# Kernel tuning notes

Hardware: AMD Instinct MI355X
Metric: run time of the kernel (lower is better)

Reference implementation:

```python
import jax, jax.numpy as jnp
import numpy as np

BN_EPS = 1e-5


def conv1x1(x, w, b):
    # x: [B, C, H, W], w: [O, C], b: [O]
    return jnp.einsum('bchw,oc->bohw', x, w) + b[None, :, None, None]


def cca(x, wq, bq, wk, bk, wv, bv, wg, bg):
    # Criss-cross attention block: full HWxHW attention with qk dim = C//8
    B, C, H, W = x.shape
    N = H * W
    q = conv1x1(x, wq, bq).reshape(B, -1, N)   # [B, C//8, N]
    k = conv1x1(x, wk, bk).reshape(B, -1, N)   # [B, C//8, N]
    v = conv1x1(x, wv, bv).reshape(B, C, N)    # [B, C, N]
    att = jax.nn.softmax(jnp.einsum('bdq,bdk->bqk', q, k), axis=-1)  # [B, N, N]
    out = jnp.einsum('bck,bqk->bcq', v, att).reshape(B, C, H, W)
    return x + conv1x1(out, wg, bg)


def setup_inputs() -> dict:
    key = jax.random.key(0)
    ks = iter(jax.random.split(key, 64))

    def rn(shape, s=0.1):
        return jax.random.normal(next(ks), shape, dtype=jnp.float32) * s

    C_IN = [48, 96, 192, 384]
    OC = 8            # hardcoded out_channels in the module
    NOUT = 19         # num_outputs
    LC = OC * 4       # last_inp_channels
    d = {}
    d['x0'] = rn((2, 48, 96, 96), 1.0)
    d['x1'] = rn((2, 96, 48, 48), 1.0)
    d['x2'] = rn((2, 192, 24, 24), 1.0)
    d['x3'] = rn((2, 384, 12, 12), 1.0)
    for i, c in enumerate(C_IN):
        d[f'w{i}'] = rn((OC, c))
        d[f'b{i}'] = rn((OC,))
    # cca3 params are never used by the original forward (it calls cca1 on x_3),
    # so only cca0/cca1/cca2 are materialized.
    for i in range(3):
        d[f'cca{i}_wq'] = rn((OC // 8, OC)); d[f'cca{i}_bq'] = rn((OC // 8,))
        d[f'cca{i}_wk'] = rn((OC // 8, OC)); d[f'cca{i}_bk'] = rn((OC // 8,))
        d[f'cca{i}_wv'] = rn((OC, OC));      d[f'cca{i}_bv'] = rn((OC,))
        d[f'cca{i}_wg'] = rn((OC, OC));      d[f'cca{i}_bg'] = rn((OC,))
    d['wl0'] = rn((LC, LC)); d['bl0'] = rn((LC,))
    d['bn_s'] = jnp.ones((LC,), jnp.float32)
    d['bn_b'] = jnp.zeros((LC,), jnp.float32)
    d['bn_m'] = rn((LC,), 0.01)
    d['bn_v'] = jnp.ones((LC,), jnp.float32)
    d['wl1'] = rn((NOUT, LC)); d['bl1'] = rn((NOUT,))
    return d


def reference(x0, x1, x2, x3, w0, b0, w1, b1, w2, b2, w3, b3,
              cca0_wq, cca0_bq, cca0_wk, cca0_bk, cca0_wv, cca0_bv, cca0_wg, cca0_bg,
              cca1_wq, cca1_bq, cca1_wk, cca1_bk, cca1_wv, cca1_bv, cca1_wg, cca1_bg,
              cca2_wq, cca2_bq, cca2_wk, cca2_bk, cca2_wv, cca2_bv, cca2_wg, cca2_bg,
              wl0, bl0, bn_s, bn_b, bn_m, bn_v, wl1, bl1):
    y0 = cca(conv1x1(x0, w0, b0), cca0_wq, cca0_bq, cca0_wk, cca0_bk, cca0_wv, cca0_bv, cca0_wg, cca0_bg)
    y1 = cca(conv1x1(x1, w1, b1), cca1_wq, cca1_bq, cca1_wk, cca1_bk, cca1_wv, cca1_bv, cca1_wg, cca1_bg)
    y2 = cca(conv1x1(x2, w2, b2), cca2_wq, cca2_bq, cca2_wk, cca2_bk, cca2_wv, cca2_bv, cca2_wg, cca2_bg)
    # NOTE: original torch code applies cca1 (not cca3) to x_3 -- reproduced faithfully.
    y3 = cca(conv1x1(x3, w3, b3), cca1_wq, cca1_bq, cca1_wk, cca1_bk, cca1_wv, cca1_bv, cca1_wg, cca1_bg)

    B, C, H0, W0 = y0.shape

    def up(t):
        # torch F.interpolate(mode='bilinear', align_corners=False) == jax half-pixel bilinear
        return jax.image.resize(t, (t.shape[0], t.shape[1], H0, W0), method='bilinear')

    x = jnp.concatenate([y0, up(y1), up(y2), up(y3)], axis=1)  # [B, 32, H0, W0]
    x = conv1x1(x, wl0, bl0)
    scale = (bn_s / jnp.sqrt(bn_v + BN_EPS))[None, :, None, None]
    x = (x - bn_m[None, :, None, None]) * scale + bn_b[None, :, None, None]
    x = jax.nn.relu(x)
    return conv1x1(x, wl1, bl1)
```

## Files before the change

### kernel.cpp

```cpp
#include <hip/hip_runtime.h>
#include <math.h>

#define LB __launch_bounds__(256)

#define NSLOT 24480
#define MT 28
#define NMOM 252
#define NBLK_Q 540
#define NSLICE 4

typedef float f32x4 __attribute__((ext_vector_type(4)));

struct QkvmArgs {
  const float *x0, *x1, *x2, *x3;
  const float *w0, *w1, *w2, *w3;
  const float *c0, *c1, *c2, *c3;
  const float *wq[4], *bq[4], *wk[4], *bk[4], *wv[4], *bv[4];
  float *P, *Q;
  float *MOMP;
};

template<int CG>
__device__ __forceinline__ void qkvm_body(const QkvmArgs& a, const int scale, const int C,
    const int N, const int slotoff, const int rel,
    const float* __restrict__ xp, const float* __restrict__ wp, const float* __restrict__ bp,
    float* s_w, float* s_sm, float* s_red, float* s_kp, float* s_v) {
  constexpr int PX = 256 / CG;
  const int tid = threadIdx.x;
  const int bpb = N / PX;
  const int b = rel / bpb, blk = rel - b*bpb;
  const int px = tid & (PX - 1), cg = tid / PX;
  const int n = blk*PX + px;
  const float* xb = xp + (size_t)b*C*N + n;
  const int c0 = cg*12;
  float xv[12];
  #pragma unroll
  for (int cc = 0; cc < 12; ++cc) xv[cc] = xb[(size_t)(c0+cc)*N];

  for (int i = tid; i < 8*C; i += 256) { const int c = i >> 3, o = i & 7; s_w[i] = wp[o*C + c]; }
  if (tid >= 128 && tid < 192) { const int t = tid - 128; s_sm[32 + t] = a.wv[scale][(t & 7)*8 + (t >> 3)]; }
  if (tid < 8) {
    s_sm[tid]      = bp[tid];
    s_sm[8 + tid]  = a.wq[scale][tid];
    s_sm[16 + tid] = a.wk[scale][tid];
    s_sm[24 + tid] = a.bv[scale][tid];
  }
  if (tid == 96) { s_sm[96] = a.bq[scale][0]; s_sm[97] = a.bk[scale][0]; }
  __syncthreads();

  float p[8];
  #pragma unroll
  for (int o = 0; o < 8; ++o) p[o] = 0.f;
  #pragma unroll
  for (int cc = 0; cc < 12; ++cc) {
    const float x = xv[cc];
    #pragma unroll
    for (int o = 0; o < 8; ++o) p[o] = fmaf(s_w[(c0+cc)*8+o], x, p[o]);
  }
  f32x4* sp = (f32x4*)&s_red[tid*8];
  sp[0] = (f32x4){p[0], p[1], p[2], p[3]};
  sp[1] = (f32x4){p[4], p[5], p[6], p[7]};
  __syncthreads();

  if (tid < PX) {
    float pc[8];
    #pragma unroll
    for (int o = 0; o < 8; ++o) {
      float s = s_sm[o];
      #pragma unroll
      for (int g = 0; g < CG; ++g) s += s_red[(g*PX + tid)*8 + o];
      pc[o] = s;
    }
    float q = s_sm[96], kv = s_sm[97];
    #pragma unroll
    for (int c = 0; c < 8; ++c) { q = fmaf(s_sm[8+c], pc[c], q); kv = fmaf(s_sm[16+c], pc[c], kv); }
    float v[8];
    #pragma unroll
    for (int o = 0; o < 8; ++o) v[o] = s_sm[24 + o];
    #pragma unroll
    for (int c = 0; c < 8; ++c) {
      const float pcc = pc[c];
      #pragma unroll
      for (int o = 0; o < 8; ++o) v[o] = fmaf(s_sm[32 + c*8 + o], pcc, v[o]);
    }
    const int g = slotoff + b*N + n;
    f32x4* Pp = (f32x4*)&a.P[(size_t)g*8];
    Pp[0] = (f32x4){pc[0], pc[1], pc[2], pc[3]};
    Pp[1] = (f32x4){pc[4], pc[5], pc[6], pc[7]};
    a.Q[g] = q;
    s_kp[tid*MT] = 1.f;
    float pw = 1.f;
    #pragma unroll
    for (int m = 1; m < MT; ++m) { pw *= kv; s_kp[tid*MT + m] = pw; }
    #pragma unroll
    for (int j = 0; j < 8; ++j) s_v[tid*8 + j] = v[j];
  }
  __syncthreads();

  if (tid < NMOM) {
    const int m = tid / 9, j = tid - m*9;
    float acc = 0.f;
    if (j == 0) {
      #pragma unroll 8
      for (int e = 0; e < PX; ++e) acc += s_kp[e*MT + m];
    } else {
      #pragma unroll 8
      for (int e = 0; e < PX; ++e) acc = fmaf(s_kp[e*MT + m], s_v[e*8 + (j-1)], acc);
    }
    a.MOMP[(size_t)blockIdx.x*NMOM + tid] = acc;
  }
}

__global__ LB void qkvm_kernel(QkvmArgs a) {
  __shared__ __align__(16) float s_w[3072];
  __shared__ __align__(16) float s_sm[104];
  __shared__ __align__(16) float s_red[256*8];
  __shared__ __align__(16) float s_kp[64*MT];
  __shared__ __align__(16) float s_v[64*8];
  const int bid = blockIdx.x;
  if (bid < 288)      qkvm_body<4> (a, 0, 48,  9216, 0,     bid,     a.x0, a.w0, a.c0, s_w, s_sm, s_red, s_kp, s_v);
  else if (bid < 432) qkvm_body<8> (a, 1, 96,  2304, 18432, bid-288, a.x1, a.w1, a.c1, s_w, s_sm, s_red, s_kp, s_v);
  else if (bid < 504) qkvm_body<16>(a, 2, 192, 576,  23040, bid-432, a.x2, a.w2, a.c2, s_w, s_sm, s_red, s_kp, s_v);
  else                qkvm_body<32>(a, 3, 384, 144,  24192, bid-504, a.x3, a.w3, a.c3, s_w, s_sm, s_red, s_kp, s_v);
}

__global__ LB void momred_kernel(const float* __restrict__ MOMP, float* __restrict__ MOMQ) {
  const int sb = blockIdx.x / NSLICE, sl = blockIdx.x - sb*NSLICE;
  const int tid = threadIdx.x;
  if (tid >= NMOM) return;
  const int start[8] = {0, 144, 288, 360, 432, 468, 504, 522};
  const int cnt[8]   = {144, 144, 72, 72, 36, 36, 18, 18};
  const int r0 = start[sb] + (cnt[sb]*sl)/NSLICE;
  const int r1 = start[sb] + (cnt[sb]*(sl+1))/NSLICE;
  const float* bp = MOMP + (size_t)r0*NMOM + tid;
  const int c = r1 - r0;
  float a0=0.f,a1=0.f,a2=0.f,a3=0.f,a4=0.f,a5=0.f,a6=0.f,a7=0.f;
  int t = 0;
  for (; t + 8 <= c; t += 8) {
    a0 += bp[(size_t)(t+0)*NMOM];
    a1 += bp[(size_t)(t+1)*NMOM];
    a2 += bp[(size_t)(t+2)*NMOM];
    a3 += bp[(size_t)(t+3)*NMOM];
    a4 += bp[(size_t)(t+4)*NMOM];
    a5 += bp[(size_t)(t+5)*NMOM];
    a6 += bp[(size_t)(t+6)*NMOM];
    a7 += bp[(size_t)(t+7)*NMOM];
  }
  for (; t < c; ++t) a0 += bp[(size_t)t*NMOM];
  const float s = ((a0+a1)+(a2+a3)) + ((a4+a5)+(a6+a7));
  MOMQ[(size_t)blockIdx.x*NMOM + tid] = s;
}

__device__ __forceinline__ void taylor_eval(const float* __restrict__ mb, const float* __restrict__ wg,
                                            const float* __restrict__ bg8, const float q,
                                            const float* __restrict__ Pp, float* y) {
  float t = 1.f, den = 0.f;
  float num[8];
  #pragma unroll
  for (int c = 0; c < 8; ++c) num[c] = 0.f;
  #pragma unroll
  for (int m = 0; m < MT; ++m) {
    const f32x4 a0 = *(const f32x4*)&mb[m*12];
    const f32x4 a1 = *(const f32x4*)&mb[m*12 + 4];
    const f32x4 a2 = *(const f32x4*)&mb[m*12 + 8];
    den    = fmaf(t, a0.x, den);
    num[0] = fmaf(t, a0.y, num[0]); num[1] = fmaf(t, a0.z, num[1]); num[2] = fmaf(t, a0.w, num[2]);
    num[3] = fmaf(t, a1.x, num[3]); num[4] = fmaf(t, a1.y, num[4]); num[5] = fmaf(t, a1.z, num[5]);
    num[6] = fmaf(t, a1.w, num[6]); num[7] = fmaf(t, a2.x, num[7]);
    if (m + 1 < MT) t *= q * (1.f/(float)(m+1));
  }
  const float inv = 1.f/den;
  float o8[8];
  #pragma unroll
  for (int c = 0; c < 8; ++c) o8[c] = num[c]*inv;
  const f32x4 pA = *(const f32x4*)Pp;
  const f32x4 pB = *(const f32x4*)(Pp + 4);
  const float pv[8] = {pA.x, pA.y, pA.z, pA.w, pB.x, pB.y, pB.z, pB.w};
  #pragma unroll
  for (int o = 0; o < 8; ++o) {
    float s2 = pv[o] + bg8[o];
    #pragma unroll
    for (int c = 0; c < 8; ++c) s2 = fmaf(wg[o*8 + c], o8[c], s2);
    y[o] = s2;
  }
}

template<int HS>
__device__ __forceinline__ void bilerp_lds(float* zo, const float* __restrict__ sYb,
                                           const int r, const int h, const int w) {
  constexpr float inv = (float)HS/96.0f;
  const float sy = (h + 0.5f)*inv - 0.5f;
  const float sx = (w + 0.5f)*inv - 0.5f;
  const int iy0 = (int)floorf(sy); const float fy = sy - (float)iy0;
  const int ix0 = (int)floorf(sx); const float fx = sx - (float)ix0;
  const float syE = (2*r + 0.5f)*inv - 0.5f;
  const int ybase = (int)floorf(syE);
  const int ly0 = iy0 - ybase;
  const int x0 = min(max(ix0, 0), HS-1), x1 = min(max(ix0 + 1, 0), HS-1);
  const float* p00 = &sYb[((ly0  )*HS + x0)*8];
  const float* p01 = &sYb[((ly0  )*HS + x1)*8];
  const float* p10 = &sYb[((ly0+1)*HS + x0)*8];
  const float* p11 = &sYb[((ly0+1)*HS + x1)*8];
  const float w00 = (1.f-fy)*(1.f-fx), w01 = (1.f-fy)*fx, w10 = fy*(1.f-fx), w11 = fy*fx;
  #pragma unroll
  for (int c = 0; c < 8; ++c)
    zo[c] = w00*p00[c] + w01*p01[c] + w10*p10[c] + w11*p11[c];
}

struct HFArgs {
  const float *Q, *P, *MOMQ;
  const float *wg0, *bg0, *wg1, *bg1, *wg2, *bg2;
  const float *wl0, *bl0, *bn_s, *bn_b, *bn_m, *bn_v, *wl1, *bl1;
  float *out;
};

__global__ LB void headfin_kernel(HFArgs a) {
  __shared__ __align__(16) float smom[8*MT*12];
  __shared__ __align__(16) float sY[2016];
  __shared__ float swg[3][64], sbg[3][8];
  __shared__ float s_wl0[1024], s_wl1[608];
  __shared__ float s_bl0[32], s_sc[32], s_sh[32], s_bl1[19];
  const int tid = threadIdx.x;
  const int bid = blockIdx.x;
  const int b = bid / 48, r = bid - b*48;

  for (int i = tid; i < 1024; i += 256) s_wl0[i] = a.wl0[i];
  for (int i = tid; i < 608;  i += 256) s_wl1[i] = a.wl1[i];
  if (tid < 64) { swg[0][tid] = a.wg0[tid]; swg[1][tid] = a.wg1[tid]; swg[2][tid] = a.wg2[tid]; }
  if (tid < 8)  { sbg[0][tid] = a.bg0[tid]; sbg[1][tid] = a.bg1[tid]; sbg[2][tid] = a.bg2[tid]; }
  if (tid >= 64 && tid < 96) {
    const int c = tid - 64;
    s_bl0[c] = a.bl0[c];
    const float sc = a.bn_s[c] / sqrtf(a.bn_v[c] + 1e-5f);
    s_sc[c] = sc;
    s_sh[c] = a.bn_b[c] - a.bn_m[c]*sc;
  }
  if (tid >= 96 && tid < 115) s_bl1[tid - 96] = a.bl1[tid - 96];
  for (int i = tid; i < 8*MT*12; i += 256) {
    const int sbi = i / (MT*12), rr = i - sbi*(MT*12);
    const int m = rr / 12, j = rr - m*12;
    float s = 0.f;
    if (j < 9) {
      const float* qp = a.MOMQ + (size_t)sbi*NSLICE*NMOM + (m*9 + j);
      #pragma unroll
      for (int sl = 0; sl < NSLICE; ++sl) s += qp[(size_t)sl*NMOM];
    }
    smom[i] = s;
  }
  __syncthreads();

  if (tid < 252) {
    int HS, soff, Nc, sb, widx, base, row_i, x;
    if (tid < 144)      { HS=48; soff=18432; Nc=2304; sb=2+b; widx=1; base=0;    row_i=tid/48;       x=tid-48*(tid/48); }
    else if (tid < 216) { const int t=tid-144; HS=24; soff=23040; Nc=576; sb=4+b; widx=2; base=1152; row_i=t/24; x=t-24*(t/24); }
    else                { const int t=tid-216; HS=12; soff=24192; Nc=144; sb=6+b; widx=1; base=1728; row_i=t/12; x=t-12*(t/12); }
    const float syE = (2*r + 0.5f)*(float)HS/96.0f - 0.5f;
    const int ybase = (int)floorf(syE);
    const int row = min(max(ybase + row_i, 0), HS-1);
    const int slot = soff + b*Nc + row*HS + x;
    float y[8];
    taylor_eval(&smom[sb*(MT*12)], swg[widx], sbg[widx], a.Q[slot], &a.P[(size_t)slot*8], y);
    #pragma unroll
    for (int c = 0; c < 8; ++c) sY[base + (row_i*HS + x)*8 + c] = y[c];
  }
  __syncthreads();

  if (tid < 192) {
    const int hh = tid / 96;
    const int h = 2*r + hh;
    const int w = tid - 96*hh;
    const int n = h*96 + w;
    float z[32];
    {
      const int slot = b*9216 + n;
      taylor_eval(&smom[b*(MT*12)], swg[0], sbg[0], a.Q[slot], &a.P[(size_t)slot*8], z);
    }
    bilerp_lds<48>(z + 8,  &sY[0],    r, h, w);
    bilerp_lds<24>(z + 16, &sY[1152], r, h, w);
    bilerp_lds<12>(z + 24, &sY[1728], r, h, w);
    float o19[19];
    #pragma unroll
    for (int j = 0; j < 19; ++j) o19[j] = s_bl1[j];
    #pragma unroll 1
    for (int o = 0; o < 32; ++o) {
      float sA = s_bl0[o], sB = 0.f;
      #pragma unroll
      for (int c4 = 0; c4 < 4; ++c4) {
        const f32x4 wv = *(const f32x4*)&s_wl0[o*32 + c4*4];
        sA = fmaf(wv.x, z[c4*4+0], sA);
        sA = fmaf(wv.y, z[c4*4+1], sA);
        sA = fmaf(wv.z, z[c4*4+2], sA);
        sA = fmaf(wv.w, z[c4*4+3], sA);
      }
      #pragma unroll
      for (int c4 = 4; c4 < 8; ++c4) {
        const f32x4 wv = *(const f32x4*)&s_wl0[o*32 + c4*4];
        sB = fmaf(wv.x, z[c4*4+0], sB);
        sB = fmaf(wv.y, z[c4*4+1], sB);
        sB = fmaf(wv.z, z[c4*4+2], sB);
        sB = fmaf(wv.w, z[c4*4+3], sB);
      }
      const float t = fmaxf(fmaf(sA + sB, s_sc[o], s_sh[o]), 0.f);
      #pragma unroll
      for (int j = 0; j < 19; ++j) o19[j] = fmaf(s_wl1[j*32 + o], t, o19[j]);
    }
    #pragma unroll
    for (int j = 0; j < 19; ++j)
      a.out[((size_t)b*19 + j)*9216 + n] = o19[j];
  }
}

extern "C" void kernel_launch(void* const* d_in, const int* in_sizes, int n_in,
                              void* d_out, int out_size, void* d_ws, size_t ws_size,
                              hipStream_t stream) {
  (void)in_sizes; (void)n_in; (void)out_size; (void)ws_size;
  const float* wq[3]; const float* bq[3]; const float* wk[3]; const float* bk[3];
  const float* wv[3]; const float* bv[3]; const float* wg[3]; const float* bg[3];
  for (int i = 0; i < 3; ++i) {
    const int base = 12 + i*8;
    wq[i] = (const float*)d_in[base + 0]; bq[i] = (const float*)d_in[base + 1];
    wk[i] = (const float*)d_in[base + 2]; bk[i] = (const float*)d_in[base + 3];
    wv[i] = (const float*)d_in[base + 4]; bv[i] = (const float*)d_in[base + 5];
    wg[i] = (const float*)d_in[base + 6]; bg[i] = (const float*)d_in[base + 7];
  }
  const int m4[4] = {0, 1, 2, 1};

  float* ws = (float*)d_ws;
  float* P = ws;
  float* Q = P + (size_t)NSLOT*8;
  float* MOMP = Q + NSLOT;
  float* MOMQ = MOMP + (size_t)NBLK_Q*NMOM;

  QkvmArgs qa;
  qa.x0 = (const float*)d_in[0]; qa.x1 = (const float*)d_in[1];
  qa.x2 = (const float*)d_in[2]; qa.x3 = (const float*)d_in[3];
  qa.w0 = (const float*)d_in[4];  qa.c0 = (const float*)d_in[5];
  qa.w1 = (const float*)d_in[6];  qa.c1 = (const float*)d_in[7];
  qa.w2 = (const float*)d_in[8];  qa.c2 = (const float*)d_in[9];
  qa.w3 = (const float*)d_in[10]; qa.c3 = (const float*)d_in[11];
  for (int s = 0; s < 4; ++s) {
    qa.wq[s] = wq[m4[s]]; qa.bq[s] = bq[m4[s]];
    qa.wk[s] = wk[m4[s]]; qa.bk[s] = bk[m4[s]];
    qa.wv[s] = wv[m4[s]]; qa.bv[s] = bv[m4[s]];
  }
  qa.P = P; qa.Q = Q; qa.MOMP = MOMP;

  HFArgs ha;
  ha.Q = Q; ha.P = P; ha.MOMQ = MOMQ;
  ha.wg0 = wg[0]; ha.bg0 = bg[0];
  ha.wg1 = wg[1]; ha.bg1 = bg[1];
  ha.wg2 = wg[2]; ha.bg2 = bg[2];
  ha.wl0 = (const float*)d_in[36]; ha.bl0 = (const float*)d_in[37];
  ha.bn_s = (const float*)d_in[38]; ha.bn_b = (const float*)d_in[39];
  ha.bn_m = (const float*)d_in[40]; ha.bn_v = (const float*)d_in[41];
  ha.wl1 = (const float*)d_in[42]; ha.bl1 = (const float*)d_in[43];
  ha.out = (float*)d_out;

  qkvm_kernel<<<NBLK_Q, 256, 0, stream>>>(qa);
  momred_kernel<<<8*NSLICE, 256, 0, stream>>>(MOMP, MOMQ);
  headfin_kernel<<<96, 256, 0, stream>>>(ha);
}
```

Baseline: 32.98 us.

## Replace shared-memory partial-sum reduction with warp shuffles in qkvm kernel

Thread mapping changes so the channel groups for one pixel sit in adjacent lanes. Their 8-channel partial sums are then reduced with xor shuffles instead of a shared-memory buffer and an extra barrier. The weight load becomes coalesced and unrolled with compile-time C, and the moment accumulation uses four independent accumulators to break the FMA dependency chain. In exchange, the x loads become strided across adjacent lanes (each lane reads a different channel block), which can hurt global-load coalescing.

```diff
diff --git a/kernel.cpp b/kernel.cpp
--- a/kernel.cpp
+++ b/kernel.cpp
@@ -21,23 +21,26 @@
 };
 
 template<int CG>
-__device__ __forceinline__ void qkvm_body(const QkvmArgs& a, const int scale, const int C,
+__device__ __forceinline__ void qkvm_body(const QkvmArgs& a, const int scale,
     const int N, const int slotoff, const int rel,
     const float* __restrict__ xp, const float* __restrict__ wp, const float* __restrict__ bp,
-    float* s_w, float* s_sm, float* s_red, float* s_kp, float* s_v) {
+    float* s_w, float* s_sm, float* s_kp, float* s_v) {
+  constexpr int C = 12 * CG;
   constexpr int PX = 256 / CG;
   const int tid = threadIdx.x;
+  const int cg = tid & (CG - 1);
+  const int pxl = tid / CG;
   const int bpb = N / PX;
   const int b = rel / bpb, blk = rel - b*bpb;
-  const int px = tid & (PX - 1), cg = tid / PX;
-  const int n = blk*PX + px;
+  const int n = blk*PX + pxl;
   const float* xb = xp + (size_t)b*C*N + n;
   const int c0 = cg*12;
   float xv[12];
   #pragma unroll
   for (int cc = 0; cc < 12; ++cc) xv[cc] = xb[(size_t)(c0+cc)*N];
 
-  for (int i = tid; i < 8*C; i += 256) { const int c = i >> 3, o = i & 7; s_w[i] = wp[o*C + c]; }
+  #pragma unroll
+  for (int j = tid; j < 8*C; j += 256) { const int o = j / C, c = j - o*C; s_w[c*8 + o] = wp[j]; }
   if (tid >= 128 && tid < 192) { const int t = tid - 128; s_sm[32 + t] = a.wv[scale][(t & 7)*8 + (t >> 3)]; }
   if (tid < 8) {
     s_sm[tid]      = bp[tid];
@@ -57,20 +60,16 @@
     #pragma unroll
     for (int o = 0; o < 8; ++o) p[o] = fmaf(s_w[(c0+cc)*8+o], x, p[o]);
   }
-  f32x4* sp = (f32x4*)&s_red[tid*8];
-  sp[0] = (f32x4){p[0], p[1], p[2], p[3]};
-  sp[1] = (f32x4){p[4], p[5], p[6], p[7]};
-  __syncthreads();
-
-  if (tid < PX) {
+  #pragma unroll
+  for (int off = 1; off < CG; off <<= 1) {
+    #pragma unroll
+    for (int o = 0; o < 8; ++o) p[o] += __shfl_xor(p[o], off);
+  }
+
+  if (cg == 0) {
     float pc[8];
     #pragma unroll
-    for (int o = 0; o < 8; ++o) {
-      float s = s_sm[o];
-      #pragma unroll
-      for (int g = 0; g < CG; ++g) s += s_red[(g*PX + tid)*8 + o];
-      pc[o] = s;
-    }
+    for (int o = 0; o < 8; ++o) pc[o] = p[o] + s_sm[o];
     float q = s_sm[96], kv = s_sm[97];
     #pragma unroll
     for (int c = 0; c < 8; ++c) { q = fmaf(s_sm[8+c], pc[c], q); kv = fmaf(s_sm[16+c], pc[c], kv); }
@@ -88,40 +87,49 @@
     Pp[0] = (f32x4){pc[0], pc[1], pc[2], pc[3]};
     Pp[1] = (f32x4){pc[4], pc[5], pc[6], pc[7]};
     a.Q[g] = q;
-    s_kp[tid*MT] = 1.f;
+    s_kp[pxl*MT] = 1.f;
     float pw = 1.f;
     #pragma unroll
-    for (int m = 1; m < MT; ++m) { pw *= kv; s_kp[tid*MT + m] = pw; }
-    #pragma unroll
-    for (int j = 0; j < 8; ++j) s_v[tid*8 + j] = v[j];
+    for (int m = 1; m < MT; ++m) { pw *= kv; s_kp[pxl*MT + m] = pw; }
+    #pragma unroll
+    for (int j = 0; j < 8; ++j) s_v[pxl*8 + j] = v[j];
   }
   __syncthreads();
 
   if (tid < NMOM) {
     const int m = tid / 9, j = tid - m*9;
-    float acc = 0.f;
+    float a0=0.f, a1=0.f, a2=0.f, a3=0.f;
     if (j == 0) {
-      #pragma unroll 8
-      for (int e = 0; e < PX; ++e) acc += s_kp[e*MT + m];
+      #pragma unroll 4
+      for (int e = 0; e < PX; e += 4) {
+        a0 += s_kp[(e+0)*MT + m];
+        a1 += s_kp[(e+1)*MT + m];
+        a2 += s_kp[(e+2)*MT + m];
+        a3 += s_kp[(e+3)*MT + m];
+      }
     } else {
-      #pragma unroll 8
-      for (int e = 0; e < PX; ++e) acc = fmaf(s_kp[e*MT + m], s_v[e*8 + (j-1)], acc);
-    }
-    a.MOMP[(size_t)blockIdx.x*NMOM + tid] = acc;
+      #pragma unroll 4
+      for (int e = 0; e < PX; e += 4) {
+        a0 = fmaf(s_kp[(e+0)*MT + m], s_v[(e+0)*8 + (j-1)], a0);
+        a1 = fmaf(s_kp[(e+1)*MT + m], s_v[(e+1)*8 + (j-1)], a1);
+        a2 = fmaf(s_kp[(e+2)*MT + m], s_v[(e+2)*8 + (j-1)], a2);
+        a3 = fmaf(s_kp[(e+3)*MT + m], s_v[(e+3)*8 + (j-1)], a3);
+      }
+    }
+    a.MOMP[(size_t)blockIdx.x*NMOM + tid] = (a0 + a1) + (a2 + a3);
   }
 }
 
 __global__ LB void qkvm_kernel(QkvmArgs a) {
   __shared__ __align__(16) float s_w[3072];
   __shared__ __align__(16) float s_sm[104];
-  __shared__ __align__(16) float s_red[256*8];
   __shared__ __align__(16) float s_kp[64*MT];
   __shared__ __align__(16) float s_v[64*8];
   const int bid = blockIdx.x;
-  if (bid < 288)      qkvm_body<4> (a, 0, 48,  9216, 0,     bid,     a.x0, a.w0, a.c0, s_w, s_sm, s_red, s_kp, s_v);
-  else if (bid < 432) qkvm_body<8> (a, 1, 96,  2304, 18432, bid-288, a.x1, a.w1, a.c1, s_w, s_sm, s_red, s_kp, s_v);
-  else if (bid < 504) qkvm_body<16>(a, 2, 192, 576,  23040, bid-432, a.x2, a.w2, a.c2, s_w, s_sm, s_red, s_kp, s_v);
-  else                qkvm_body<32>(a, 3, 384, 144,  24192, bid-504, a.x3, a.w3, a.c3, s_w, s_sm, s_red, s_kp, s_v);
+  if (bid < 288)      qkvm_body<4> (a, 0, 9216, 0,     bid,     a.x0, a.w0, a.c0, s_w, s_sm, s_kp, s_v);
+  else if (bid < 432) qkvm_body<8> (a, 1, 2304, 18432, bid-288, a.x1, a.w1, a.c1, s_w, s_sm, s_kp, s_v);
+  else if (bid < 504) qkvm_body<16>(a, 2, 576,  23040, bid-432, a.x2, a.w2, a.c2, s_w, s_sm, s_kp, s_v);
+  else                qkvm_body<32>(a, 3, 144,  24192, bid-504, a.x3, a.w3, a.c3, s_w, s_sm, s_kp, s_v);
 }
 
 __global__ LB void momred_kernel(const float* __restrict__ MOMP, float* __restrict__ MOMQ) {
```

Result: slower. 35.57 us (+7.8%).
